# Optimization experiments

Measured on AMD Instinct MI355X. Metric: run time of the kernel, lower is better.

Reference implementation:

```python
import jax, jax.numpy as jnp
import numpy as np

FEAT = 4      # feature_dim
INFO = 8      # info_dim
B, U, A = 128, 16, 1024  # batch, num_users, num_ris_antennas


def setup_inputs() -> dict:
    key = jax.random.key(0)
    ks = jax.random.split(key, 7)
    channel = jax.random.normal(ks[0], (B, FEAT, U, A), dtype=jnp.float32)
    # layer 1: four branches (ll, lg, gl, gg), each Conv2d(4, 8, 1) -> W:[Cin,Cout]
    W1 = jax.random.normal(ks[1], (4, FEAT, INFO), dtype=jnp.float32) * 0.3
    b1 = jax.random.normal(ks[2], (4, INFO), dtype=jnp.float32) * 0.01
    # layers 2..7: four branches each Conv2d(32, 8, 1)
    Wm = jax.random.normal(ks[3], (6, 4, 4 * INFO, INFO), dtype=jnp.float32) * 0.15
    bm = jax.random.normal(ks[4], (6, 4, INFO), dtype=jnp.float32) * 0.01
    # layer 8: Conv2d(32, 1, 1)
    W8 = jax.random.normal(ks[5], (4 * INFO, 1), dtype=jnp.float32) * 0.15
    b8 = jax.random.normal(ks[6], (1,), dtype=jnp.float32) * 0.01
    return {"channel": channel, "W1": W1, "b1": b1, "Wm": Wm, "bm": bm,
            "W8": W8, "b8": b8}


def _conv1x1(x, W, b):
    # x: [B, Cin, U, A], W: [Cin, Cout], b: [Cout]
    return jnp.einsum('bcua,co->boua', x, W) + b[None, :, None, None]


def _process(x, W, b, e_u, e_a):
    # W: [4, Cin, INFO], b: [4, INFO]; branches: ll, lg, gl, gg
    f_ll = jax.nn.relu(_conv1x1(x, W[0], b[0]))
    f_lg = jnp.einsum('boua,ax->boux', jax.nn.relu(_conv1x1(x, W[1], b[1])), e_a)
    f_gl = jnp.einsum('uv,bova->boua', e_u, jax.nn.relu(_conv1x1(x, W[2], b[2])))
    gg = jnp.einsum('uv,bova->boua', e_u, jax.nn.relu(_conv1x1(x, W[3], b[3])))
    f_gg = jnp.einsum('boua,ax->boux', gg, e_a)
    return jnp.concatenate([f_ll, f_lg, f_gl, f_gg], axis=1)


def reference(channel, W1, b1, Wm, bm, W8, b8):
    _, _, nu, na = channel.shape
    # global_info flags True -> uniform averaging matrices ones/N
    e_u = jnp.full((nu, nu), 1.0 / nu, dtype=channel.dtype)
    e_a = jnp.full((na, na), 1.0 / na, dtype=channel.dtype)

    f = _process(channel, W1, b1, e_u, e_a)
    f1 = f                                      # skip 1
    f = _process(f, Wm[0], bm[0], e_u, e_a)     # layer 2
    f = _process(f, Wm[1], bm[1], e_u, e_a)     # layer 3
    f3 = f                                      # skip 3
    f = _process(f, Wm[2], bm[2], e_u, e_a)     # layer 4
    f = _process(f, Wm[3], bm[3], e_u, e_a)     # layer 5
    f = (f + f1) / 2
    f = _process(f, Wm[4], bm[4], e_u, e_a)     # layer 6
    f = _process(f, Wm[5], bm[5], e_u, e_a)     # layer 7
    f = (f + f3) / 2
    out = _conv1x1(f, W8, b8).mean(axis=2) * jnp.pi   # mean over users -> [B, 1, A]
    return out
```

## Files before the change

kernel.cpp:

```cpp
#include <hip/hip_runtime.h>


#define NB 128
#define NU 16
#define NA 1024

typedef float v2f __attribute__((ext_vector_type(2)));
typedef __attribute__((ext_vector_type(8))) short bf16x8;
typedef __attribute__((ext_vector_type(16))) float f32x16;

static constexpr float PI_F = 3.14159265358979323846f;

__device__ __forceinline__ void pk_fma_acc(v2f& acc, v2f a, v2f b) {
    asm("v_pk_fma_f32 %0, %1, %2, %0" : "+v"(acc) : "v"(a), "v"(b));
}
__device__ __forceinline__ unsigned int cvtpk(float a, float b) {
    unsigned int r;
    asm("v_cvt_pk_bf16_f32 %0, %1, %2" : "=v"(r) : "v"(a), "v"(b));
    return r;
}
__device__ __forceinline__ void unpack8(uint4 v, float x[8]) {
    x[0] = __uint_as_float(v.x << 16); x[1] = __uint_as_float(v.x & 0xffff0000u);
    x[2] = __uint_as_float(v.y << 16); x[3] = __uint_as_float(v.y & 0xffff0000u);
    x[4] = __uint_as_float(v.z << 16); x[5] = __uint_as_float(v.z & 0xffff0000u);
    x[6] = __uint_as_float(v.w << 16); x[7] = __uint_as_float(v.w & 0xffff0000u);
}
__device__ __forceinline__ void store8f(unsigned short* p, const float y[8]) {
    uint4 v;
    v.x = cvtpk(y[0], y[1]); v.y = cvtpk(y[2], y[3]);
    v.z = cvtpk(y[4], y[5]); v.w = cvtpk(y[6], y[7]);
    *reinterpret_cast<uint4*>(p) = v;
}
__device__ __forceinline__ float treesum16(f32x16 v) {
    float a0 = v[0] + v[1], a1 = v[2] + v[3], a2 = v[4] + v[5], a3 = v[6] + v[7];
    float a4 = v[8] + v[9], a5 = v[10] + v[11], a6 = v[12] + v[13], a7 = v[14] + v[15];
    float b0 = a0 + a1, b1 = a2 + a3, b2 = a4 + a5, b3 = a6 + a7;
    return (b0 + b1) + (b2 + b3);
}

__device__ __forceinline__ float merge3v(const v2f* y, int lane) {
    float w[4];
    const bool s0 = (lane & 1) != 0;
#pragma unroll
    for (int k = 0; k < 4; ++k) {
        float lo = s0 ? y[k].y : y[k].x;
        float hi = s0 ? y[k].x : y[k].y;
        w[k] = lo + __shfl_xor(hi, 1, 64);
    }
    const bool s1 = (lane & 2) != 0;
#pragma unroll
    for (int k = 0; k < 2; ++k) {
        float lo = s1 ? w[2 * k + 1] : w[2 * k];
        float hi = s1 ? w[2 * k] : w[2 * k + 1];
        w[k] = lo + __shfl_xor(hi, 2, 64);
    }
    const bool s2 = (lane & 4) != 0;
    float lo = s2 ? w[1] : w[0];
    float hi = s2 ? w[0] : w[1];
    return lo + __shfl_xor(hi, 4, 64);
}

template <int NZ>
__global__ __launch_bounds__(128) void layer_first_t(
    const float* __restrict__ ch, const float* __restrict__ W1,
    const float* __restrict__ b1, unsigned short* __restrict__ ll_out,
    float* __restrict__ lg_out, float* __restrict__ gl_out,
    float* __restrict__ gg_out)
{
    constexpr int UN = NU / NZ;
    const int b = blockIdx.x;
    const int a = blockIdx.y * 128 + threadIdx.x;
    const int uz = blockIdx.z;
    const int lane = threadIdx.x & 63;
    const int tid = threadIdx.x;

    __shared__ float s_lg[UN][8];
    __shared__ float s_gg[8];
    for (int t = tid; t < UN * 8; t += 128) s_lg[t >> 3][t & 7] = 0.f;
    if (tid >= 64 && tid < 72) s_gg[tid & 7] = 0.f;
    __syncthreads();

    v2f glacc2[4], ggacc2[4];
#pragma unroll
    for (int i = 0; i < 4; ++i) { glacc2[i] = v2f{0.f, 0.f}; ggacc2[i] = v2f{0.f, 0.f}; }

#pragma unroll
    for (int k = 0; k < UN; ++k) {
        const int u = uz * UN + k;
        float x[4];
#pragma unroll
        for (int c = 0; c < 4; ++c)
            x[c] = ch[(((size_t)b * 4 + c) * NU + u) * NA + a];

        v2f y2[16];
        const v2f* b2 = reinterpret_cast<const v2f*>(b1);
#pragma unroll
        for (int o = 0; o < 16; ++o) y2[o] = b2[o];
#pragma unroll
        for (int c = 0; c < 4; ++c) {
            const v2f xx = v2f{x[c], x[c]};
#pragma unroll
            for (int j = 0; j < 4; ++j) {
                const v2f* wr = reinterpret_cast<const v2f*>(W1 + (j * 4 + c) * 8);
#pragma unroll
                for (int oi = 0; oi < 4; ++oi)
                    pk_fma_acc(y2[j * 4 + oi], xx, wr[oi]);
            }
        }
#pragma unroll
        for (int o = 0; o < 16; ++o)
            y2[o] = v2f{__builtin_fmaxf(y2[o].x, 0.f), __builtin_fmaxf(y2[o].y, 0.f)};

        const size_t xoff = (((size_t)(b * NU + u)) * NA + a) * 8;
        {
            uint4 v;
            v.x = cvtpk(y2[0].x, y2[0].y); v.y = cvtpk(y2[1].x, y2[1].y);
            v.z = cvtpk(y2[2].x, y2[2].y); v.w = cvtpk(y2[3].x, y2[3].y);
            *reinterpret_cast<uint4*>(ll_out + xoff) = v;
        }
#pragma unroll
        for (int i = 0; i < 4; ++i) {
            glacc2[i] += y2[8 + i];
            ggacc2[i] += y2[12 + i];
        }
        float lr = merge3v(y2 + 4, lane);
        atomicAdd(&s_lg[k][lane & 7], lr);
    }
    {
        const float invU = 1.f / 16.f;
        float ga[8];
#pragma unroll
        for (int i = 0; i < 4; ++i) { ga[2*i] = glacc2[i].x; ga[2*i+1] = glacc2[i].y; }
#pragma unroll
        for (int c = 0; c < 8; ++c)
            gl_out[(((size_t)uz * NB + b) * 8 + c) * NA + a] = ga[c] * invU;
    }
    float gga[8];
#pragma unroll
    for (int i = 0; i < 4; ++i) { gga[2*i] = ggacc2[i].x; gga[2*i+1] = ggacc2[i].y; }
    float gr = merge3v(reinterpret_cast<const v2f*>(gga), lane);
    atomicAdd(&s_gg[lane & 7], gr);
    __syncthreads();
    for (int t = tid; t < UN * 8; t += 128)
        atomicAdd(lg_out + ((size_t)b * NU + uz * UN + (t >> 3)) * 8 + (t & 7),
                  s_lg[t >> 3][t & 7]);
    if (tid >= 64 && tid < 72)
        atomicAdd(gg_out + b * 8 + (tid & 7), s_gg[tid & 7]);
}

__global__ __launch_bounds__(256) void prep_base_k(
    const float* __restrict__ lg_sum, const float* __restrict__ lg_skip,
    const float* __restrict__ gg_sum, const float* __restrict__ gg_skip,
    const float* __restrict__ Wl, const float* __restrict__ bl,
    float* __restrict__ base)
{
    const int t = blockIdx.x * 256 + threadIdx.x;
    if (t >= NB * NU) return;
    const int b = t >> 4;
    const float invA = 1.f / 1024.f, invUA = 1.f / 16384.f;
    float lg[8], gg[8];
#pragma unroll
    for (int c = 0; c < 8; ++c) {
        float v = lg_sum[t * 8 + c] * invA;
        if (lg_skip) v = (v + lg_skip[t * 8 + c] * invA) * 0.5f;
        lg[c] = v;
    }
#pragma unroll
    for (int c = 0; c < 8; ++c) {
        float v = gg_sum[b * 8 + c] * invUA;
        if (gg_skip) v = (v + gg_skip[b * 8 + c] * invUA) * 0.5f;
        gg[c] = v;
    }
    float y[32];
#pragma unroll
    for (int o = 0; o < 32; ++o) y[o] = bl[o];
#pragma unroll
    for (int j = 0; j < 4; ++j)
#pragma unroll
        for (int c = 0; c < 8; ++c) {
            const float* wl = Wl + (j * 32 + 8 + c) * 8;
            const float* wg = Wl + (j * 32 + 24 + c) * 8;
#pragma unroll
            for (int oi = 0; oi < 8; ++oi) {
                y[j * 8 + oi] = fmaf(lg[c], wl[oi], y[j * 8 + oi]);
                y[j * 8 + oi] = fmaf(gg[c], wg[oi], y[j * 8 + oi]);
            }
        }
#pragma unroll
    for (int o = 0; o < 32; ++o) base[t * 32 + o] = y[o];
}

template <int NZ>
__global__ __launch_bounds__(64) void layer_main_t(
    const unsigned short* ll_in, const float* __restrict__ gl_in,
    const float* __restrict__ gl_skip, const float* __restrict__ base,
    const float* __restrict__ Wl,
    const unsigned short* __restrict__ ll_skip,
    const float* __restrict__ ch, const float* __restrict__ W1,
    const float* __restrict__ b1,
    unsigned short* ll_out, float* __restrict__ lg_out,
    float* __restrict__ gl_out, float* __restrict__ gg_out)
{
    constexpr int UN = NU / NZ;
    const int b = blockIdx.x;
    const int lane = threadIdx.x;
    const int o = lane & 31;
    const int h4 = 4 * (lane >> 5);
    const int half = lane >> 5;
    const int a32 = blockIdx.y * 32 + o;
    const int uz = blockIdx.z;
    const bool lohalf = lane < 32;

    __shared__ float s_lg[UN][8];
    __shared__ float s_gg[8];
    __shared__ float myl[8 * 68];
    for (int t = lane; t < UN * 8; t += 64) s_lg[t >> 3][t & 7] = 0.f;
    if (lane < 8) s_gg[lane] = 0.f;
    __syncthreads();

    const int jbr = o >> 3, oi = o & 7;

    bf16x8 Bfrag;
    {
        unsigned int t4[4];
#pragma unroll
        for (int r = 0; r < 4; ++r) {
            float w0 = Wl[(jbr * 32 + 2 * r) * 8 + oi];
            float w1 = Wl[(jbr * 32 + 2 * r + 1) * 8 + oi];
            float h0 = __uint_as_float(cvtpk(w0, w0) << 16);
            float h1 = __uint_as_float(cvtpk(w1, w1) << 16);
            t4[r] = cvtpk(lohalf ? w0 : (w0 - h0), lohalf ? w1 : (w1 - h1));
        }
        uint4 bw = make_uint4(t4[0], t4[1], t4[2], t4[3]);
        Bfrag = __builtin_bit_cast(bf16x8, bw);
    }

    float g[8];
#pragma unroll
    for (int c = 0; c < 8; ++c) {
        float s = 0.f;
#pragma unroll
        for (int z = 0; z < NZ; ++z)
            s += gl_in[(((size_t)z * NB + b) * 8 + c) * NA + a32];
        g[c] = s;
    }
    if (gl_skip) {
#pragma unroll
        for (int c = 0; c < 8; ++c) {
            float s = 0.f;
#pragma unroll
            for (int z = 0; z < NZ; ++z)
                s += gl_skip[(((size_t)z * NB + b) * 8 + c) * NA + a32];
            g[c] = (g[c] + s) * 0.5f;
        }
    }

    f32x16 cT;
    {
        bf16x8 Ag, Bh, Br;
        {
            unsigned int t4[4];
#pragma unroll
            for (int r = 0; r < 4; ++r) {
                float g0 = g[2 * r], g1 = g[2 * r + 1];
                float h0 = __uint_as_float(cvtpk(g0, g0) << 16);
                float h1 = __uint_as_float(cvtpk(g1, g1) << 16);
                t4[r] = cvtpk(lohalf ? g0 : (g0 - h0), lohalf ? g1 : (g1 - h1));
            }
            uint4 u = make_uint4(t4[0], t4[1], t4[2], t4[3]);
            Ag = __builtin_bit_cast(bf16x8, u);
        }
        {
            unsigned int th[4], tr[4];
#pragma unroll
            for (int r = 0; r < 4; ++r) {
                float w0 = Wl[(jbr * 32 + 16 + 2 * r) * 8 + oi];
                float w1 = Wl[(jbr * 32 + 16 + 2 * r + 1) * 8 + oi];
                float h0 = __uint_as_float(cvtpk(w0, w0) << 16);
                float h1 = __uint_as_float(cvtpk(w1, w1) << 16);
                th[r] = cvtpk(w0, w1);
                tr[r] = cvtpk(w0 - h0, w1 - h1);
            }
            uint4 uh = make_uint4(th[0], th[1], th[2], th[3]);
            uint4 ur = make_uint4(tr[0], tr[1], tr[2], tr[3]);
            Bh = __builtin_bit_cast(bf16x8, uh);
            Br = __builtin_bit_cast(bf16x8, ur);
        }
        f32x16 z16;
#pragma unroll
        for (int r = 0; r < 16; ++r) z16[r] = 0.f;
        cT = __builtin_amdgcn_mfma_f32_32x32x16_bf16(Ag, Bh, z16, 0, 0, 0);
        cT = __builtin_amdgcn_mfma_f32_32x32x16_bf16(Ag, Br, cT, 0, 0, 0);
    }

    f32x16 acc;
#pragma unroll
    for (int r = 0; r < 16; ++r) acc[r] = 0.f;

    const unsigned short* llrow =
        ll_in + (((size_t)(b * NU + uz * UN + half)) * NA + a32) * 8;
    const size_t pstride = (size_t)2 * NA * 8;
    uint4 xv = *reinterpret_cast<const uint4*>(llrow);

#pragma unroll
    for (int kp = 0; kp < UN / 2; ++kp) {
        const int u0 = uz * UN + 2 * kp;
        uint4 xnext = xv;
        if (kp + 1 < UN / 2)
            xnext = *reinterpret_cast<const uint4*>(llrow + (size_t)(kp + 1) * pstride);

        const float bse0 = base[(b * NU + u0) * 32 + o];
        const float bse1 = base[(b * NU + u0 + 1) * 32 + o];

        uint4 xs;
        xs.x = (unsigned)__shfl_xor((int)xv.x, 32, 64);
        xs.y = (unsigned)__shfl_xor((int)xv.y, 32, 64);
        xs.z = (unsigned)__shfl_xor((int)xv.z, 32, 64);
        xs.w = (unsigned)__shfl_xor((int)xv.w, 32, 64);
        uint4 a0u, a1u;
        a0u.x = lohalf ? xv.x : xs.x; a0u.y = lohalf ? xv.y : xs.y;
        a0u.z = lohalf ? xv.z : xs.z; a0u.w = lohalf ? xv.w : xs.w;
        a1u.x = lohalf ? xs.x : xv.x; a1u.y = lohalf ? xs.y : xv.y;
        a1u.z = lohalf ? xs.z : xv.z; a1u.w = lohalf ? xs.w : xv.w;
        bf16x8 A0 = __builtin_bit_cast(bf16x8, a0u);
        bf16x8 A1 = __builtin_bit_cast(bf16x8, a1u);

        f32x16 d0 = __builtin_amdgcn_mfma_f32_32x32x16_bf16(A0, Bfrag, cT, 0, 0, 0);
        f32x16 d1 = __builtin_amdgcn_mfma_f32_32x32x16_bf16(A1, Bfrag, cT, 0, 0, 0);
#pragma unroll
        for (int r = 0; r < 16; ++r) {
            d0[r] = __builtin_fmaxf(d0[r] + bse0, 0.f);
            d1[r] = __builtin_fmaxf(d1[r] + bse1, 0.f);
        }

        float red0 = treesum16(d0);
        red0 += __shfl_xor(red0, 32, 64);
        if (lane >= 8 && lane < 16) atomicAdd(&s_lg[2 * kp][lane - 8], red0);
        float red1 = treesum16(d1);
        red1 += __shfl_xor(red1, 32, 64);
        if (lane >= 8 && lane < 16) atomicAdd(&s_lg[2 * kp + 1][lane - 8], red1);

#pragma unroll
        for (int r = 0; r < 16; ++r) acc[r] += d0[r] + d1[r];

        if (o < 8) {
#pragma unroll
            for (int q = 0; q < 4; ++q) {
                *reinterpret_cast<float4*>(&myl[o * 68 + q * 8 + h4]) =
                    make_float4(d0[4*q], d0[4*q+1], d0[4*q+2], d0[4*q+3]);
                *reinterpret_cast<float4*>(&myl[o * 68 + 32 + q * 8 + h4]) =
                    make_float4(d1[4*q], d1[4*q+1], d1[4*q+2], d1[4*q+3]);
            }
        }
        __syncthreads();
        float y[8];
#pragma unroll
        for (int c = 0; c < 8; ++c) y[c] = myl[c * 68 + lane];

        const int u_lane = u0 + half;
        const size_t xoff = (((size_t)(b * NU + u_lane)) * NA + a32) * 8;
        if (ll_skip) {
            float s[8];
            unpack8(*reinterpret_cast<const uint4*>(ll_skip + xoff), s);
#pragma unroll
            for (int c = 0; c < 8; ++c) y[c] = (y[c] + s[c]) * 0.5f;
        } else if (ch) {
            float xc[4];
#pragma unroll
            for (int c = 0; c < 4; ++c)
                xc[c] = ch[(((size_t)b * 4 + c) * NU + u_lane) * NA + a32];
            float s[8];
#pragma unroll
            for (int i = 0; i < 8; ++i) s[i] = b1[i];
#pragma unroll
            for (int c = 0; c < 4; ++c)
#pragma unroll
                for (int i = 0; i < 8; ++i)
                    s[i] = fmaf(xc[c], W1[c * 8 + i], s[i]);
#pragma unroll
            for (int i = 0; i < 8; ++i)
                y[i] = (y[i] + __builtin_fmaxf(s[i], 0.f)) * 0.5f;
        }
        store8f(ll_out + xoff, y);
        __syncthreads();
        xv = xnext;
    }

    float gr = treesum16(acc);
    gr += __shfl_xor(gr, 32, 64);
    if (lane >= 24 && lane < 32) atomicAdd(&s_gg[lane - 24], gr);

    if (o >= 16 && o < 24) {
        const float invU = 1.f / 16.f;
        float* gp = gl_out + (((size_t)uz * NB + b) * 8 + (o - 16)) * NA
                  + blockIdx.y * 32;
#pragma unroll
        for (int q = 0; q < 4; ++q)
            *reinterpret_cast<float4*>(gp + q * 8 + h4) =
                make_float4(acc[4*q]*invU, acc[4*q+1]*invU, acc[4*q+2]*invU, acc[4*q+3]*invU);
    }
    __syncthreads();
    for (int t = lane; t < UN * 8; t += 64)
        atomicAdd(lg_out + ((size_t)b * NU + uz * UN + (t >> 3)) * 8 + (t & 7),
                  s_lg[t >> 3][t & 7]);
    if (lane < 8)
        atomicAdd(gg_out + b * 8 + lane, s_gg[lane]);
}

template <int NZ>
__global__ __launch_bounds__(128) void layer_out_t(
    const unsigned short* __restrict__ ll,
    const float* __restrict__ lg7, const float* __restrict__ lg3,
    const float* __restrict__ gl7, const float* __restrict__ gl3,
    const float* __restrict__ gg7, const float* __restrict__ gg3,
    const float* __restrict__ W8, const float* __restrict__ b8,
    float* __restrict__ out)
{
    constexpr int UN = NU / NZ;
    const int b = blockIdx.x;
    const int a = blockIdx.y * 128 + threadIdx.x;
    const int uz = blockIdx.z;
    const float invA = 1.f / 1024.f, invUA = 1.f / 16384.f, invU = 1.f / 16.f;

    float acc = 0.f;
#pragma unroll
    for (int k = 0; k < UN; ++k) {
        const int u = uz * UN + k;
        float x[8];
        unpack8(*reinterpret_cast<const uint4*>(
            ll + (((size_t)(b * NU + u)) * NA + a) * 8), x);
#pragma unroll
        for (int c = 0; c < 8; ++c) acc += x[c] * W8[c];
    }
    acc *= invU;

    if (uz == 0) {
        float sb = b8[0];
#pragma unroll
        for (int c = 0; c < 8; ++c) {
            float s7 = 0.f, s3 = 0.f;
#pragma unroll
            for (int u = 0; u < NU; ++u) {
                s7 += lg7[(b * NU + u) * 8 + c];
                s3 += lg3[(b * NU + u) * 8 + c];
            }
            sb += ((s7 * invA + s3 * invA) * 0.5f * invU) * W8[8 + c];
        }
#pragma unroll
        for (int c = 0; c < 8; ++c)
            sb += ((gg7[b * 8 + c] + gg3[b * 8 + c]) * invUA * 0.5f) * W8[24 + c];

        float s7[8], s3[8];
#pragma unroll
        for (int i = 0; i < 8; ++i) { s7[i] = 0.f; s3[i] = 0.f; }
#pragma unroll
        for (int z = 0; z < NZ; ++z)
#pragma unroll
            for (int i = 0; i < 8; ++i) {
                s7[i] += gl7[(((size_t)z * NB + b) * 8 + i) * NA + a];
                s3[i] += gl3[(((size_t)z * NB + b) * 8 + i) * NA + a];
            }
#pragma unroll
        for (int i = 0; i < 8; ++i)
            acc += 0.5f * (s7[i] + s3[i]) * W8[16 + i];
        acc += sb;
    }
    atomicAdd(out + (size_t)b * NA + a, acc * PI_F);
}

static constexpr size_t LLsz = (size_t)NB * NU * NA * 8;
static constexpr size_t GLsz = (size_t)NB * NA * 8;
static constexpr size_t LGsz = (size_t)NB * NU * 8;
static constexpr size_t GGsz = (size_t)NB * 8;

template <int NZ>
static void run_pipeline(const float* channel, const float* W1, const float* b1,
                         const float* Wm, const float* bm, const float* W8,
                         const float* b8, float* out, int out_bytes,
                         void* d_ws, hipStream_t stream)
{
    unsigned short* cur = (unsigned short*)d_ws;
    unsigned short* f3s = cur + LLsz;
    float* glb = (float*)(f3s + LLsz);
    float* g0 = glb;
    float* g1 = glb + (size_t)NZ * GLsz;
    float* g2 = glb + (size_t)2 * NZ * GLsz;
    float* g3 = glb + (size_t)3 * NZ * GLsz;
    float* lgb = glb + (size_t)4 * NZ * GLsz;
    float* ggb = lgb + 7 * LGsz;
    float* base = ggb + 7 * GGsz;

    hipMemsetAsync(lgb, 0, (7 * LGsz + 7 * GGsz) * sizeof(float), stream);
    hipMemsetAsync(out, 0, out_bytes, stream);

    dim3 gridF(NB, NA / 128, NZ), blkF(128);
    dim3 gridM(NB, NA / 32, NZ), blkM(64);

    layer_first_t<NZ><<<gridF, blkF, 0, stream>>>(channel, W1, b1, cur, lgb, g0, ggb);

    prep_base_k<<<8, 256, 0, stream>>>(lgb, nullptr, ggb, nullptr, Wm, bm, base);
    layer_main_t<NZ><<<gridM, blkM, 0, stream>>>(cur, g0, nullptr, base, Wm,
        nullptr, nullptr, nullptr, nullptr,
        cur, lgb + 1 * LGsz, g2, ggb + 1 * GGsz);

    prep_base_k<<<8, 256, 0, stream>>>(lgb + 1 * LGsz, nullptr, ggb + 1 * GGsz, nullptr,
                                       Wm + 1024, bm + 32, base);
    layer_main_t<NZ><<<gridM, blkM, 0, stream>>>(cur, g2, nullptr, base, Wm + 1024,
        nullptr, nullptr, nullptr, nullptr,
        f3s, lgb + 2 * LGsz, g1, ggb + 2 * GGsz);

    prep_base_k<<<8, 256, 0, stream>>>(lgb + 2 * LGsz, nullptr, ggb + 2 * GGsz, nullptr,
                                       Wm + 2048, bm + 64, base);
    layer_main_t<NZ><<<gridM, blkM, 0, stream>>>(f3s, g1, nullptr, base, Wm + 2048,
        nullptr, nullptr, nullptr, nullptr,
        cur, lgb + 3 * LGsz, g3, ggb + 3 * GGsz);

    prep_base_k<<<8, 256, 0, stream>>>(lgb + 3 * LGsz, nullptr, ggb + 3 * GGsz, nullptr,
                                       Wm + 3072, bm + 96, base);
    layer_main_t<NZ><<<gridM, blkM, 0, stream>>>(cur, g3, nullptr, base, Wm + 3072,
        nullptr, channel, W1, b1,
        cur, lgb + 4 * LGsz, g2, ggb + 4 * GGsz);

    prep_base_k<<<8, 256, 0, stream>>>(lgb + 4 * LGsz, lgb, ggb + 4 * GGsz, ggb,
                                       Wm + 4096, bm + 128, base);
    layer_main_t<NZ><<<gridM, blkM, 0, stream>>>(cur, g2, g0, base, Wm + 4096,
        nullptr, nullptr, nullptr, nullptr,
        cur, lgb + 5 * LGsz, g3, ggb + 5 * GGsz);

    prep_base_k<<<8, 256, 0, stream>>>(lgb + 5 * LGsz, nullptr, ggb + 5 * GGsz, nullptr,
                                       Wm + 5120, bm + 160, base);
    layer_main_t<NZ><<<gridM, blkM, 0, stream>>>(cur, g3, nullptr, base, Wm + 5120,
        f3s, nullptr, nullptr, nullptr,
        cur, lgb + 6 * LGsz, g2, ggb + 6 * GGsz);

    layer_out_t<NZ><<<gridF, blkF, 0, stream>>>(cur, lgb + 6 * LGsz, lgb + 2 * LGsz,
                                                g2, g1, ggb + 6 * GGsz, ggb + 2 * GGsz,
                                                W8, b8, out);
}

static size_t ws_req(int nz) {
    return LLsz * 2 * sizeof(unsigned short)
         + (size_t)4 * nz * GLsz * sizeof(float)
         + (7 * LGsz + 7 * GGsz + 2048 * 32) * sizeof(float);
}

extern "C" void kernel_launch(void* const* d_in, const int* in_sizes, int n_in,
                              void* d_out, int out_size, void* d_ws, size_t ws_size,
                              hipStream_t stream) {
    const float* channel = (const float*)d_in[0];
    const float* W1 = (const float*)d_in[1];
    const float* b1 = (const float*)d_in[2];
    const float* Wm = (const float*)d_in[3];
    const float* bm = (const float*)d_in[4];
    const float* W8 = (const float*)d_in[5];
    const float* b8 = (const float*)d_in[6];
    float* out = (float*)d_out;

    if (ws_size >= ws_req(2)) {
        run_pipeline<2>(channel, W1, b1, Wm, bm, W8, b8, out, out_size, d_ws, stream);
    } else {
        run_pipeline<1>(channel, W1, b1, Wm, bm, W8, b8, out, out_size, d_ws, stream);
    }
}
```

Before: 331.8 us.

## Fuse base prep into main layer kernel and fold final W8 projection into last layer

```diff
diff --git a/kernel.cpp b/kernel.cpp
--- a/kernel.cpp
+++ b/kernel.cpp
@@ -18,6 +18,9 @@
     unsigned int r;
     asm("v_cvt_pk_bf16_f32 %0, %1, %2" : "=v"(r) : "v"(a), "v"(b));
     return r;
+}
+__device__ __forceinline__ float bf16hi(float x) {
+    return __uint_as_float(cvtpk(x, x) << 16);
 }
 __device__ __forceinline__ void unpack8(uint4 v, float x[8]) {
     x[0] = __uint_as_float(v.x << 16); x[1] = __uint_as_float(v.x & 0xffff0000u);
@@ -148,58 +151,19 @@
         atomicAdd(gg_out + b * 8 + (tid & 7), s_gg[tid & 7]);
 }
 
-__global__ __launch_bounds__(256) void prep_base_k(
-    const float* __restrict__ lg_sum, const float* __restrict__ lg_skip,
-    const float* __restrict__ gg_sum, const float* __restrict__ gg_skip,
-    const float* __restrict__ Wl, const float* __restrict__ bl,
-    float* __restrict__ base)
-{
-    const int t = blockIdx.x * 256 + threadIdx.x;
-    if (t >= NB * NU) return;
-    const int b = t >> 4;
-    const float invA = 1.f / 1024.f, invUA = 1.f / 16384.f;
-    float lg[8], gg[8];
-#pragma unroll
-    for (int c = 0; c < 8; ++c) {
-        float v = lg_sum[t * 8 + c] * invA;
-        if (lg_skip) v = (v + lg_skip[t * 8 + c] * invA) * 0.5f;
-        lg[c] = v;
-    }
-#pragma unroll
-    for (int c = 0; c < 8; ++c) {
-        float v = gg_sum[b * 8 + c] * invUA;
-        if (gg_skip) v = (v + gg_skip[b * 8 + c] * invUA) * 0.5f;
-        gg[c] = v;
-    }
-    float y[32];
-#pragma unroll
-    for (int o = 0; o < 32; ++o) y[o] = bl[o];
-#pragma unroll
-    for (int j = 0; j < 4; ++j)
-#pragma unroll
-        for (int c = 0; c < 8; ++c) {
-            const float* wl = Wl + (j * 32 + 8 + c) * 8;
-            const float* wg = Wl + (j * 32 + 24 + c) * 8;
-#pragma unroll
-            for (int oi = 0; oi < 8; ++oi) {
-                y[j * 8 + oi] = fmaf(lg[c], wl[oi], y[j * 8 + oi]);
-                y[j * 8 + oi] = fmaf(gg[c], wg[oi], y[j * 8 + oi]);
-            }
-        }
-#pragma unroll
-    for (int o = 0; o < 32; ++o) base[t * 32 + o] = y[o];
-}
-
 template <int NZ>
 __global__ __launch_bounds__(64) void layer_main_t(
     const unsigned short* ll_in, const float* __restrict__ gl_in,
-    const float* __restrict__ gl_skip, const float* __restrict__ base,
-    const float* __restrict__ Wl,
+    const float* __restrict__ gl_skip,
+    const float* __restrict__ lg_in, const float* __restrict__ lg_skip,
+    const float* __restrict__ gg_in, const float* __restrict__ gg_skip,
+    const float* __restrict__ Wl, const float* __restrict__ bl,
     const unsigned short* __restrict__ ll_skip,
     const float* __restrict__ ch, const float* __restrict__ W1,
     const float* __restrict__ b1,
     unsigned short* ll_out, float* __restrict__ lg_out,
-    float* __restrict__ gl_out, float* __restrict__ gg_out)
+    float* __restrict__ gl_out, float* __restrict__ gg_out,
+    const float* __restrict__ W8v, float* __restrict__ out_part)
 {
     constexpr int UN = NU / NZ;
     const int b = blockIdx.x;
@@ -210,6 +174,7 @@
     const int a32 = blockIdx.y * 32 + o;
     const int uz = blockIdx.z;
     const bool lohalf = lane < 32;
+    const float invA = 1.f / 1024.f, invUA = 1.f / 16384.f;
 
     __shared__ float s_lg[UN][8];
     __shared__ float s_gg[8];
@@ -227,12 +192,22 @@
         for (int r = 0; r < 4; ++r) {
             float w0 = Wl[(jbr * 32 + 2 * r) * 8 + oi];
             float w1 = Wl[(jbr * 32 + 2 * r + 1) * 8 + oi];
-            float h0 = __uint_as_float(cvtpk(w0, w0) << 16);
-            float h1 = __uint_as_float(cvtpk(w1, w1) << 16);
+            float h0 = bf16hi(w0), h1 = bf16hi(w1);
             t4[r] = cvtpk(lohalf ? w0 : (w0 - h0), lohalf ? w1 : (w1 - h1));
         }
         uint4 bw = make_uint4(t4[0], t4[1], t4[2], t4[3]);
         Bfrag = __builtin_bit_cast(bf16x8, bw);
+    }
+
+    float Wlg[8];
+#pragma unroll
+    for (int c = 0; c < 8; ++c) Wlg[c] = Wl[(jbr * 32 + 8 + c) * 8 + oi];
+    float base_c = bl[o];
+#pragma unroll
+    for (int c = 0; c < 8; ++c) {
+        float v = gg_in[b * 8 + c] * invUA;
+        if (gg_skip) v = (v + gg_skip[b * 8 + c] * invUA) * 0.5f;
+        base_c = fmaf(v, Wl[(jbr * 32 + 24 + c) * 8 + oi], base_c);
     }
 
     float g[8];
@@ -263,8 +238,7 @@
 #pragma unroll
             for (int r = 0; r < 4; ++r) {
                 float g0 = g[2 * r], g1 = g[2 * r + 1];
-                float h0 = __uint_as_float(cvtpk(g0, g0) << 16);
-                float h1 = __uint_as_float(cvtpk(g1, g1) << 16);
+                float h0 = bf16hi(g0), h1 = bf16hi(g1);
                 t4[r] = cvtpk(lohalf ? g0 : (g0 - h0), lohalf ? g1 : (g1 - h1));
             }
             uint4 u = make_uint4(t4[0], t4[1], t4[2], t4[3]);
@@ -276,8 +250,7 @@
             for (int r = 0; r < 4; ++r) {
                 float w0 = Wl[(jbr * 32 + 16 + 2 * r) * 8 + oi];
                 float w1 = Wl[(jbr * 32 + 16 + 2 * r + 1) * 8 + oi];
-                float h0 = __uint_as_float(cvtpk(w0, w0) << 16);
-                float h1 = __uint_as_float(cvtpk(w1, w1) << 16);
+                float h0 = bf16hi(w0), h1 = bf16hi(w1);
                 th[r] = cvtpk(w0, w1);
                 tr[r] = cvtpk(w0 - h0, w1 - h1);
             }
@@ -296,6 +269,7 @@
     f32x16 acc;
 #pragma unroll
     for (int r = 0; r < 16; ++r) acc[r] = 0.f;
+    float p8 = 0.f;
 
     const unsigned short* llrow =
         ll_in + (((size_t)(b * NU + uz * UN + half)) * NA + a32) * 8;
@@ -309,8 +283,26 @@
         if (kp + 1 < UN / 2)
             xnext = *reinterpret_cast<const uint4*>(llrow + (size_t)(kp + 1) * pstride);
 
-        const float bse0 = base[(b * NU + u0) * 32 + o];
-        const float bse1 = base[(b * NU + u0 + 1) * 32 + o];
+        float bse0 = base_c, bse1 = base_c;
+        {
+            const float* l0 = lg_in + (b * NU + u0) * 8;
+            const float* l1 = l0 + 8;
+            if (lg_skip) {
+                const float* s0 = lg_skip + (b * NU + u0) * 8;
+                const float* s1 = s0 + 8;
+#pragma unroll
+                for (int c = 0; c < 8; ++c) {
+                    bse0 = fmaf((l0[c] * invA + s0[c] * invA) * 0.5f, Wlg[c], bse0);
+                    bse1 = fmaf((l1[c] * invA + s1[c] * invA) * 0.5f, Wlg[c], bse1);
+                }
+            } else {
+#pragma unroll
+                for (int c = 0; c < 8; ++c) {
+                    bse0 = fmaf(l0[c] * invA, Wlg[c], bse0);
+                    bse1 = fmaf(l1[c] * invA, Wlg[c], bse1);
+                }
+            }
+        }
 
         uint4 xs;
         xs.x = (unsigned)__shfl_xor((int)xv.x, 32, 64);
@@ -381,9 +373,21 @@
             for (int i = 0; i < 8; ++i)
                 y[i] = (y[i] + __builtin_fmaxf(s[i], 0.f)) * 0.5f;
         }
-        store8f(ll_out + xoff, y);
+        if (W8v) {
+            float d = 0.f;
+#pragma unroll
+            for (int c = 0; c < 8; ++c) d = fmaf(y[c], W8v[c], d);
+            p8 += d;
+        } else {
+            store8f(ll_out + xoff, y);
+        }
         __syncthreads();
         xv = xnext;
+    }
+
+    if (W8v) {
+        p8 += __shfl_xor(p8, 32, 64);
+        if (lohalf) atomicAdd(&out_part[(size_t)b * NA + a32], p8);
     }
 
     float gr = treesum16(acc);
@@ -408,64 +412,46 @@
 }
 
 template <int NZ>
-__global__ __launch_bounds__(128) void layer_out_t(
-    const unsigned short* __restrict__ ll,
+__global__ __launch_bounds__(128) void layer_out_fin(
+    const float* __restrict__ outp,
     const float* __restrict__ lg7, const float* __restrict__ lg3,
     const float* __restrict__ gl7, const float* __restrict__ gl3,
     const float* __restrict__ gg7, const float* __restrict__ gg3,
     const float* __restrict__ W8, const float* __restrict__ b8,
     float* __restrict__ out)
 {
-    constexpr int UN = NU / NZ;
     const int b = blockIdx.x;
     const int a = blockIdx.y * 128 + threadIdx.x;
-    const int uz = blockIdx.z;
     const float invA = 1.f / 1024.f, invUA = 1.f / 16384.f, invU = 1.f / 16.f;
 
-    float acc = 0.f;
-#pragma unroll
-    for (int k = 0; k < UN; ++k) {
-        const int u = uz * UN + k;
-        float x[8];
-        unpack8(*reinterpret_cast<const uint4*>(
-            ll + (((size_t)(b * NU + u)) * NA + a) * 8), x);
-#pragma unroll
-        for (int c = 0; c < 8; ++c) acc += x[c] * W8[c];
-    }
-    acc *= invU;
-
-    if (uz == 0) {
-        float sb = b8[0];
-#pragma unroll
-        for (int c = 0; c < 8; ++c) {
-            float s7 = 0.f, s3 = 0.f;
-#pragma unroll
-            for (int u = 0; u < NU; ++u) {
-                s7 += lg7[(b * NU + u) * 8 + c];
-                s3 += lg3[(b * NU + u) * 8 + c];
-            }
-            sb += ((s7 * invA + s3 * invA) * 0.5f * invU) * W8[8 + c];
-        }
-#pragma unroll
-        for (int c = 0; c < 8; ++c)
-            sb += ((gg7[b * 8 + c] + gg3[b * 8 + c]) * invUA * 0.5f) * W8[24 + c];
-
-        float s7[8], s3[8];
-#pragma unroll
-        for (int i = 0; i < 8; ++i) { s7[i] = 0.f; s3[i] = 0.f; }
-#pragma unroll
-        for (int z = 0; z < NZ; ++z)
-#pragma unroll
-            for (int i = 0; i < 8; ++i) {
-                s7[i] += gl7[(((size_t)z * NB + b) * 8 + i) * NA + a];
-                s3[i] += gl3[(((size_t)z * NB + b) * 8 + i) * NA + a];
-            }
-#pragma unroll
-        for (int i = 0; i < 8; ++i)
-            acc += 0.5f * (s7[i] + s3[i]) * W8[16 + i];
-        acc += sb;
-    }
-    atomicAdd(out + (size_t)b * NA + a, acc * PI_F);
+    float acc = outp[(size_t)b * NA + a] * invU;
+
+    float sb = b8[0];
+#pragma unroll
+    for (int c = 0; c < 8; ++c) {
+        float s7 = 0.f, s3 = 0.f;
+#pragma unroll
+        for (int u = 0; u < NU; ++u) {
+            s7 += lg7[(b * NU + u) * 8 + c];
+            s3 += lg3[(b * NU + u) * 8 + c];
+        }
+        sb += ((s7 * invA + s3 * invA) * 0.5f * invU) * W8[8 + c];
+    }
+#pragma unroll
+    for (int c = 0; c < 8; ++c)
+        sb += ((gg7[b * 8 + c] + gg3[b * 8 + c]) * invUA * 0.5f) * W8[24 + c];
+
+#pragma unroll
+    for (int i = 0; i < 8; ++i) {
+        float s7 = 0.f, s3 = 0.f;
+#pragma unroll
+        for (int z = 0; z < NZ; ++z) {
+            s7 += gl7[(((size_t)z * NB + b) * 8 + i) * NA + a];
+            s3 += gl3[(((size_t)z * NB + b) * 8 + i) * NA + a];
+        }
+        acc += 0.5f * (s7 + s3) * W8[16 + i];
+    }
+    out[(size_t)b * NA + a] = (acc + sb) * PI_F;
 }
 
 static constexpr size_t LLsz = (size_t)NB * NU * NA * 8;
@@ -488,60 +474,56 @@
     float* g3 = glb + (size_t)3 * NZ * GLsz;
     float* lgb = glb + (size_t)4 * NZ * GLsz;
     float* ggb = lgb + 7 * LGsz;
-    float* base = ggb + 7 * GGsz;
-
-    hipMemsetAsync(lgb, 0, (7 * LGsz + 7 * GGsz) * sizeof(float), stream);
-    hipMemsetAsync(out, 0, out_bytes, stream);
+    float* outp = ggb + 7 * GGsz;
+
+    hipMemsetAsync(lgb, 0,
+                   (7 * LGsz + 7 * GGsz + (size_t)NB * NA) * sizeof(float), stream);
 
     dim3 gridF(NB, NA / 128, NZ), blkF(128);
     dim3 gridM(NB, NA / 32, NZ), blkM(64);
+    dim3 gridO(NB, NA / 128), blkO(128);
 
     layer_first_t<NZ><<<gridF, blkF, 0, stream>>>(channel, W1, b1, cur, lgb, g0, ggb);
 
-    prep_base_k<<<8, 256, 0, stream>>>(lgb, nullptr, ggb, nullptr, Wm, bm, base);
-    layer_main_t<NZ><<<gridM, blkM, 0, stream>>>(cur, g0, nullptr, base, Wm,
+    layer_main_t<NZ><<<gridM, blkM, 0, stream>>>(cur, g0, nullptr,
+        lgb, nullptr, ggb, nullptr, Wm, bm,
         nullptr, nullptr, nullptr, nullptr,
-        cur, lgb + 1 * LGsz, g2, ggb + 1 * GGsz);
-
-    prep_base_k<<<8, 256, 0, stream>>>(lgb + 1 * LGsz, nullptr, ggb + 1 * GGsz, nullptr,
-                                       Wm + 1024, bm + 32, base);
-    layer_main_t<NZ><<<gridM, blkM, 0, stream>>>(cur, g2, nullptr, base, Wm + 1024,
+        cur, lgb + 1 * LGsz, g2, ggb + 1 * GGsz, nullptr, nullptr);
+
+    layer_main_t<NZ><<<gridM, blkM, 0, stream>>>(cur, g2, nullptr,
+        lgb + 1 * LGsz, nullptr, ggb + 1 * GGsz, nullptr, Wm + 1024, bm + 32,
         nullptr, nullptr, nullptr, nullptr,
-        f3s, lgb + 2 * LGsz, g1, ggb + 2 * GGsz);
-
-    prep_base_k<<<8, 256, 0, stream>>>(lgb + 2 * LGsz, nullptr, ggb + 2 * GGsz, nullptr,
-                                       Wm + 2048, bm + 64, base);
-    layer_main_t<NZ><<<gridM, blkM, 0, stream>>>(f3s, g1, nullptr, base, Wm + 2048,
+        f3s, lgb + 2 * LGsz, g1, ggb + 2 * GGsz, nullptr, nullptr);
+
+    layer_main_t<NZ><<<gridM, blkM, 0, stream>>>(f3s, g1, nullptr,
+        lgb + 2 * LGsz, nullptr, ggb + 2 * GGsz, nullptr, Wm + 2048, bm + 64,
         nullptr, nullptr, nullptr, nullptr,
-        cur, lgb + 3 * LGsz, g3, ggb + 3 * GGsz);
-
-    prep_base_k<<<8, 256, 0, stream>>>(lgb + 3 * LGsz, nullptr, ggb + 3 * GGsz, nullptr,
-                                       Wm + 3072, bm + 96, base);
-    layer_main_t<NZ><<<gridM, blkM, 0, stream>>>(cur, g3, nullptr, base, Wm + 3072,
+        cur, lgb + 3 * LGsz, g3, ggb + 3 * GGsz, nullptr, nullptr);
+
+    layer_main_t<NZ><<<gridM, blkM, 0, stream>>>(cur, g3, nullptr,
+        lgb + 3 * LGsz, nullptr, ggb + 3 * GGsz, nullptr, Wm + 3072, bm + 96,
         nullptr, channel, W1, b1,
-        cur, lgb + 4 * LGsz, g2, ggb + 4 * GGsz);
-
-    prep_base_k<<<8, 256, 0, stream>>>(lgb + 4 * LGsz, lgb, ggb + 4 * GGsz, ggb,
-                                       Wm + 4096, bm + 128, base);
-    layer_main_t<NZ><<<gridM, blkM, 0, stream>>>(cur, g2, g0, base, Wm + 4096,
+        cur, lgb + 4 * LGsz, g2, ggb + 4 * GGsz, nullptr, nullptr);
+
+    layer_main_t<NZ><<<gridM, blkM, 0, stream>>>(cur, g2, g0,
+        lgb + 4 * LGsz, lgb, ggb + 4 * GGsz, ggb, Wm + 4096, bm + 128,
         nullptr, nullptr, nullptr, nullptr,
-        cur, lgb + 5 * LGsz, g3, ggb + 5 * GGsz);
-
-    prep_base_k<<<8, 256, 0, stream>>>(lgb + 5 * LGsz, nullptr, ggb + 5 * GGsz, nullptr,
-                                       Wm + 5120, bm + 160, base);
-    layer_main_t<NZ><<<gridM, blkM, 0, stream>>>(cur, g3, nullptr, base, Wm + 5120,
+        cur, lgb + 5 * LGsz, g3, ggb + 5 * GGsz, nullptr, nullptr);
+
+    layer_main_t<NZ><<<gridM, blkM, 0, stream>>>(cur, g3, nullptr,
+        lgb + 5 * LGsz, nullptr, ggb + 5 * GGsz, nullptr, Wm + 5120, bm + 160,
         f3s, nullptr, nullptr, nullptr,
-        cur, lgb + 6 * LGsz, g2, ggb + 6 * GGsz);
-
-    layer_out_t<NZ><<<gridF, blkF, 0, stream>>>(cur, lgb + 6 * LGsz, lgb + 2 * LGsz,
-                                                g2, g1, ggb + 6 * GGsz, ggb + 2 * GGsz,
-                                                W8, b8, out);
+        cur, lgb + 6 * LGsz, g2, ggb + 6 * GGsz, W8, outp);
+
+    layer_out_fin<NZ><<<gridO, blkO, 0, stream>>>(outp, lgb + 6 * LGsz, lgb + 2 * LGsz,
+                                                  g2, g1, ggb + 6 * GGsz, ggb + 2 * GGsz,
+                                                  W8, b8, out);
 }
 
 static size_t ws_req(int nz) {
     return LLsz * 2 * sizeof(unsigned short)
          + (size_t)4 * nz * GLsz * sizeof(float)
-         + (7 * LGsz + 7 * GGsz + 2048 * 32) * sizeof(float);
+         + (7 * LGsz + 7 * GGsz + (size_t)NB * NA) * sizeof(float);
 }
 
 extern "C" void kernel_launch(void* const* d_in, const int* in_sizes, int n_in,
```

Result: faster. 308.2 us (-7.1%).
